# Optimization experiments

Hardware: AMD Instinct MI355X
Metric: run time of the kernel (lower is better)

## Reference

```python
import jax, jax.numpy as jnp
import numpy as np

EPS = 1e-5  # torch BatchNorm default

def _conv(x, w, pad):
    return jax.lax.conv_general_dilated(x, w, window_strides=(1, 1), padding=pad,
                                        dimension_numbers=('NCHW', 'OIHW', 'NCHW'))

def _bn(x, g, b, m, v):
    # eval-mode BatchNorm2d over channel axis 1 of NCHW
    scale = g / jnp.sqrt(v + EPS)
    return x * scale[None, :, None, None] + (b - m * scale)[None, :, None, None]

def _bn1d(x, g, b, m, v):
    scale = g / jnp.sqrt(v + EPS)
    return x * scale[None, :] + (b - m * scale)[None, :]

def _prelu(x, a):
    # torch PReLU with num_parameters=1 (scalar slope, init 0.25)
    return jnp.where(x >= 0, x, a * x)

def setup_inputs():
    key = jax.random.key(0)
    ks = jax.random.split(key, 10)
    B, H, W = 256, 600, 19
    C1, C2 = 40, 40
    x = jax.random.normal(ks[0], (B, H, W), jnp.float32)
    w1 = jax.random.normal(ks[1], (C1, 1, 29, 1), jnp.float32) * 0.1
    w2 = jax.random.normal(ks[2], (C2, C1, 1, 19), jnp.float32) * 0.1
    fc1_w = jax.random.uniform(ks[3], (80, 1560), jnp.float32, -0.005, 0.005)
    fc2_w = jax.random.uniform(ks[4], (2, 80), jnp.float32, -0.005, 0.005)
    def bn_params(k, n):
        k1, k2 = jax.random.split(k)
        return (jnp.ones((n,), jnp.float32), jnp.zeros((n,), jnp.float32),
                jax.random.normal(k1, (n,), jnp.float32) * 0.1,
                jax.random.uniform(k2, (n,), jnp.float32, 0.5, 1.5))
    bn1_g, bn1_b, bn1_m, bn1_v = bn_params(ks[5], C1)
    bn2_g, bn2_b, bn2_m, bn2_v = bn_params(ks[6], C2)
    bn3_g, bn3_b, bn3_m, bn3_v = bn_params(ks[7], 80)
    a1 = jnp.full((1,), 0.25, jnp.float32)
    a2 = jnp.full((1,), 0.25, jnp.float32)
    a3 = jnp.full((1,), 0.25, jnp.float32)
    return dict(x=x, w1=w1, bn1_g=bn1_g, bn1_b=bn1_b, bn1_m=bn1_m, bn1_v=bn1_v, a1=a1,
                w2=w2, bn2_g=bn2_g, bn2_b=bn2_b, bn2_m=bn2_m, bn2_v=bn2_v, a2=a2,
                fc1_w=fc1_w, bn3_g=bn3_g, bn3_b=bn3_b, bn3_m=bn3_m, bn3_v=bn3_v, a3=a3,
                fc2_w=fc2_w)

def reference(x, w1, bn1_g, bn1_b, bn1_m, bn1_v, a1,
              w2, bn2_g, bn2_b, bn2_m, bn2_v, a2,
              fc1_w, bn3_g, bn3_b, bn3_m, bn3_v, a3, fc2_w):
    h = x[:, None, :, :]                                  # [B,1,600,19]
    # conv1: inputs NOT binarized, weights sign-binarized
    h = _conv(h, jnp.sign(w1), [(14, 14), (0, 0)])         # [B,40,600,19]
    h = _prelu(_bn(h, bn1_g, bn1_b, bn1_m, bn1_v), a1)
    # conv2: inputs and weights binarized
    h = _conv(jnp.sign(h), jnp.sign(w2), [(0, 0), (0, 0)])  # [B,40,600,1]
    h = _prelu(_bn(h, bn2_g, bn2_b, bn2_m, bn2_v), a2)
    # AvgPool2d kernel (30,1) stride (15,1)
    h = jax.lax.reduce_window(h, 0.0, jax.lax.add, (1, 1, 30, 1), (1, 1, 15, 1), 'VALID') / 30.0  # [B,40,39,1]
    h = h.reshape(h.shape[0], -1)                          # [B,1560]
    # fc1: binarized input/weight; BatchNorm1d; PReLU; dropout is identity in eval
    h = jnp.sign(h) @ jnp.sign(fc1_w).T                    # [B,80]
    h = _prelu(_bn1d(h, bn3_g, bn3_b, bn3_m, bn3_v), a3)
    out = jnp.sign(h) @ jnp.sign(fc2_w).T                  # [B,2]
    return out
```

## Files before the change

### kernel.cpp

```cpp
#include <hip/hip_runtime.h>
#include <stdint.h>

#define B_ 256
#define H_ 600
#define W_ 19
#define C1_ 40
#define C2_ 40
#define KH_ 29
#define PAD_ 14
#define NW_ 760
#define NWORDS_ 12
#define NJ_ 39
#define FIN_ 1560
#define FOUT_ 80
#define FCW_ 25
#define XST2 329
#define HS_ 300

__device__ __forceinline__ float fsgn(float x){ return (x > 0.f) ? 1.f : ((x < 0.f) ? -1.f : 0.f); }
__device__ __forceinline__ int8_t isgn(float x){ return (int8_t)((x > 0.f) - (x < 0.f)); }

__global__ void k0_setup(const float* __restrict__ w1, const float* __restrict__ w2,
                         const float* __restrict__ fc1w, const float* __restrict__ fc2w,
                         const float* __restrict__ g1, const float* __restrict__ b1,
                         const float* __restrict__ m1, const float* __restrict__ v1,
                         const float* __restrict__ g2, const float* __restrict__ b2,
                         const float* __restrict__ m2, const float* __restrict__ v2,
                         const float* __restrict__ g3, const float* __restrict__ b3,
                         const float* __restrict__ m3, const float* __restrict__ v3,
                         float* __restrict__ w1s, uint64_t* __restrict__ w2m,
                         uint64_t* __restrict__ fc1p, int8_t* __restrict__ fc2s,
                         float* __restrict__ bnp)
{
  int tid = blockIdx.x * blockDim.x + threadIdx.x;
  int np  = gridDim.x * blockDim.x;
  int lane = threadIdx.x & 63;
  int gw   = tid >> 6;
  int nw   = np >> 6;

  for (int i = tid; i < C1_*KH_; i += np) w1s[i] = fsgn(w1[i]);

  for (int v = gw; v < C2_*NWORDS_; v += nw){
    int c2 = v / NWORDS_, wd = v % NWORDS_;
    int idx = wd*64 + lane;
    float val = 0.f;
    if (idx < NW_){
      int c1 = idx % 40, w = idx / 40;
      val = w2[c2*NW_ + c1*W_ + w];
    }
    unsigned long long m = __ballot(val > 0.f);
    if (lane == 0) w2m[c2*NWORDS_ + wd] = m;
  }
  for (int v = gw; v < FOUT_*2*FCW_; v += nw){
    int o = v / (2*FCW_), r = v % (2*FCW_);
    int neg = r / FCW_, wd = r % FCW_;
    int e = wd*64 + lane;
    float val = (e < FIN_) ? fc1w[o*FIN_ + e] : 0.f;
    unsigned long long m = __ballot(neg ? (val < 0.f) : (val > 0.f));
    if (lane == 0) fc1p[o*(2*FCW_) + r] = m;
  }
  for (int i = tid; i < 2*FOUT_; i += np) fc2s[i] = isgn(fc2w[i]);
  for (int i = tid; i < C1_; i += np){
    float s = __fdiv_rn(g1[i], __fsqrt_rn(__fadd_rn(v1[i], 1e-5f)));
    bnp[i] = s; bnp[40+i] = __fsub_rn(b1[i], __fmul_rn(m1[i], s));
  }
  for (int i = tid; i < C2_; i += np){
    float s = __fdiv_rn(g2[i], __fsqrt_rn(__fadd_rn(v2[i], 1e-5f)));
    bnp[80+i] = s; bnp[120+i] = __fsub_rn(b2[i], __fmul_rn(m2[i], s));
  }
  for (int i = tid; i < FOUT_; i += np){
    float s = __fdiv_rn(g3[i], __fsqrt_rn(__fadd_rn(v3[i], 1e-5f)));
    bnp[160+i] = s; bnp[240+i] = __fsub_rn(b3[i], __fmul_rn(m3[i], s));
  }
}

template<int T>
__device__ __forceinline__ float acc29(float (&xw)[29], float (&wt)[29]){
  float a = 0.f;
  #pragma unroll
  for (int k = 0; k < 29; ++k)
    a = __builtin_fmaf(wt[k], xw[(T + k) % 29], a);
  return a;
}

template<int T>
__device__ __forceinline__ void step1(float (&xw)[29], float (&wt)[29],
                                      const float* xck, ulonglong2* ob,
                                      float scale, float bias, int lane){
  xw[(T + 28) % 29] = xck[T + 28];
  float acc = acc29<T>(xw, wt);
  float z = __fadd_rn(__fmul_rn(acc, scale), bias);
  unsigned long long pp = __ballot(z > 0.f);
  unsigned long long nn = __ballot(z < 0.f);
  if (lane == 0){ ulonglong2 v; v.x = pp; v.y = pp | nn; ob[T] = v; }
}

#define S1(t) step1<t>(xw, wt, xck, ob, scale, bias, lane);

__global__ __launch_bounds__(768, 6) void k1_conv1(const float* __restrict__ x,
                                                   const float* __restrict__ w1s,
                                                   const float* __restrict__ bnp,
                                                   uint64_t* __restrict__ s1bits)
{
  __shared__ float xs[W_ * XST2];
  int b = blockIdx.x, t = blockIdx.y;
  int h0 = HS_ * t;
  const float* xb = x + (size_t)b * H_ * W_;
  for (int i = threadIdx.x; i < (HS_ + 28) * W_; i += 768){
    int r = i / W_, w = i % W_;
    int gh = h0 - PAD_ + r;
    xs[w*XST2 + r] = (gh >= 0 && gh < H_) ? xb[gh*W_ + w] : 0.f;
  }
  __syncthreads();

  int tid  = threadIdx.x;
  int lane = tid & 63, wave = tid >> 6;
  bool valid = (tid < NW_);
  int c1 = tid % 40;
  int w  = valid ? (tid / 40) : 18;

  float wt[KH_];
  #pragma unroll
  for (int k = 0; k < KH_; ++k) wt[k] = w1s[c1*KH_ + k];
  float scale = bnp[c1], bias = bnp[40 + c1];
  if (!valid){ scale = __builtin_nanf(""); bias = scale; }
  const float* xcol = &xs[w * XST2];

  float xw[29];
  #pragma unroll
  for (int s = 0; s < 28; ++s) xw[s] = xcol[s];

  ulonglong2* obase = (ulonglong2*)s1bits + ((size_t)(b*12 + wave) * H_ + h0);

  #pragma unroll 1
  for (int c = 0; c < 10; ++c){
    const float* xck = xcol + 29*c;
    ulonglong2* ob = obase + 29*c;
    S1(0)  S1(1)  S1(2)  S1(3)  S1(4)  S1(5)  S1(6)  S1(7)  S1(8)  S1(9)
    S1(10) S1(11) S1(12) S1(13) S1(14) S1(15) S1(16) S1(17) S1(18) S1(19)
    S1(20) S1(21) S1(22) S1(23) S1(24) S1(25) S1(26) S1(27) S1(28)
  }
  {
    const float* xck = xcol + 290;
    ulonglong2* ob = obase + 290;
    S1(0) S1(1) S1(2) S1(3) S1(4) S1(5) S1(6) S1(7) S1(8) S1(9)
  }
}

__global__ __launch_bounds__(640) void k2_conv2pool(const uint64_t* __restrict__ s1bits,
                                                    const uint64_t* __restrict__ w2m_g,
                                                    const float* __restrict__ bnp,
                                                    const float* __restrict__ a2p,
                                                    int8_t* __restrict__ sp)
{
  __shared__ float z[C2_][640];
  int b = blockIdx.x;
  int tid = threadIdx.x;
  int rowc = (tid < H_) ? tid : (H_ - 1);

  uint64_t Pv[NWORDS_], Mv[NWORDS_];
  const ulonglong2* sb = (const ulonglong2*)s1bits + (size_t)b * NWORDS_ * H_;
  #pragma unroll
  for (int wd = 0; wd < NWORDS_; ++wd){
    ulonglong2 pm = sb[(size_t)wd * H_ + rowc];
    Pv[wd] = pm.x; Mv[wd] = pm.y;
  }
  int nzv = 0;
  #pragma unroll
  for (int wd = 0; wd < NWORDS_; ++wd) nzv += __popcll(Mv[wd]);

  float alpha = a2p[0];
  #pragma unroll 2
  for (int c2 = 0; c2 < C2_; ++c2){
    int dsum = 0;
    #pragma unroll
    for (int wd = 0; wd < NWORDS_; ++wd)
      dsum += __popcll(Mv[wd] & (Pv[wd] ^ w2m_g[c2*NWORDS_ + wd]));
    int y = nzv - 2*dsum;
    float u = __fadd_rn(__fmul_rn((float)y, bnp[c2]), bnp[40 + c2]);
    z[c2][tid] = (u >= 0.f) ? u : __fmul_rn(alpha, u);
  }
  __syncthreads();

  for (int o = tid; o < C2_*NJ_; o += 640){
    int c2 = o / NJ_, j = o % NJ_;
    float s = 0.f;
    int base = 15*j;
    #pragma unroll
    for (int r = 0; r < 30; ++r) s = __fadd_rn(s, z[c2][base + r]);
    sp[(size_t)b*FIN_ + o] = (int8_t)((s > 0.f) - (s < 0.f));
  }
}

__global__ __launch_bounds__(128) void k3_fc(const int8_t* __restrict__ sp,
                                             const uint64_t* __restrict__ fc1p,
                                             const int8_t* __restrict__ fc2s,
                                             const float* __restrict__ bnp,
                                             const float* __restrict__ a3p,
                                             float* __restrict__ out)
{
  __shared__ uint64_t spP[FCW_], spN[FCW_];
  __shared__ int z3[FOUT_];
  int b = blockIdx.x;
  int lane = threadIdx.x & 63, wave = threadIdx.x >> 6;
  const int8_t* spb = sp + (size_t)b * FIN_;
  for (int wd = wave; wd < FCW_; wd += 2){
    int e = wd*64 + lane;
    int v = (e < FIN_) ? (int)spb[e] : 0;
    unsigned long long p = __ballot(v > 0);
    unsigned long long n = __ballot(v < 0);
    if (lane == 0){ spP[wd] = p; spN[wd] = n; }
  }
  __syncthreads();
  float alpha = a3p[0];
  if (threadIdx.x < FOUT_){
    int o = threadIdx.x;
    const uint64_t* wp = fc1p + o * (2*FCW_);
    int acc = 0;
    #pragma unroll
    for (int wd = 0; wd < FCW_; ++wd){
      uint64_t P = spP[wd], N = spN[wd];
      uint64_t WP = wp[wd], WN = wp[FCW_ + wd];
      acc += __popcll(P & WP) + __popcll(N & WN) - __popcll(P & WN) - __popcll(N & WP);
    }
    float u = __fadd_rn(__fmul_rn((float)acc, bnp[o]), bnp[80 + o]);
    float z = (u >= 0.f) ? u : __fmul_rn(alpha, u);
    z3[o] = (z > 0.f) - (z < 0.f);
  }
  __syncthreads();
  if (threadIdx.x < 2){
    int k = threadIdx.x;
    int acc = 0;
    for (int o = 0; o < FOUT_; ++o) acc += z3[o] * (int)fc2s[k * FOUT_ + o];
    out[b*2 + k] = (float)acc;
  }
}

extern "C" void kernel_launch(void* const* d_in, const int* in_sizes, int n_in,
                              void* d_out, int out_size, void* d_ws, size_t ws_size,
                              hipStream_t stream)
{
  const float* x    = (const float*)d_in[0];
  const float* w1   = (const float*)d_in[1];
  const float* g1   = (const float*)d_in[2];
  const float* b1   = (const float*)d_in[3];
  const float* m1   = (const float*)d_in[4];
  const float* v1   = (const float*)d_in[5];
  const float* a1   = (const float*)d_in[6];   (void)a1;
  const float* w2   = (const float*)d_in[7];
  const float* g2   = (const float*)d_in[8];
  const float* b2   = (const float*)d_in[9];
  const float* m2   = (const float*)d_in[10];
  const float* v2   = (const float*)d_in[11];
  const float* a2   = (const float*)d_in[12];
  const float* fc1w = (const float*)d_in[13];
  const float* g3   = (const float*)d_in[14];
  const float* b3   = (const float*)d_in[15];
  const float* m3   = (const float*)d_in[16];
  const float* v3   = (const float*)d_in[17];
  const float* a3   = (const float*)d_in[18];
  const float* fc2w = (const float*)d_in[19];

  char* ws = (char*)d_ws;
  uint64_t* s1bits = (uint64_t*)(ws);
  uint64_t* w2m    = (uint64_t*)(ws + 29491200);
  float*    w1s    = (float*)   (ws + 29495040);
  float*    bnp    = (float*)   (ws + 29499680);
  int8_t*   sp     = (int8_t*)  (ws + 29500960);
  uint64_t* fc1p   = (uint64_t*)(ws + 29900320);
  int8_t*   fc2s   = (int8_t*)  (ws + 29932320);

  k0_setup<<<dim3(128), dim3(256), 0, stream>>>(w1, w2, fc1w, fc2w,
                                                g1, b1, m1, v1,
                                                g2, b2, m2, v2,
                                                g3, b3, m3, v3,
                                                w1s, w2m, fc1p, fc2s, bnp);
  k1_conv1<<<dim3(B_, 2), dim3(768), 0, stream>>>(x, w1s, bnp, s1bits);
  k2_conv2pool<<<dim3(B_), dim3(640), 0, stream>>>(s1bits, w2m, bnp + 80, a2, sp);
  k3_fc<<<dim3(B_), dim3(128), 0, stream>>>(sp, fc1p, fc2s, bnp + 160, a3, (float*)d_out);
}
```

Baseline: 219.9 us.

## Fuse conv2/pool with FC layers and retile conv1 into smaller blocks

The conv2+pool kernel and the FC kernel are merged into one, so pooled signs are packed into bitmasks via ballot in shared memory and the int8 intermediate round-trip plus a launch are removed. Conv1 is retiled from 768-thread blocks over 300-row halves into 256-thread blocks over 150-row quarters across three wave groups. This gives more, smaller blocks for occupancy at the cost of more halo reloads. Opaque asm barriers are added on loads to stop the compiler rematerialising or reordering shared and weight loads.

```diff
diff --git a/kernel.cpp b/kernel.cpp
--- a/kernel.cpp
+++ b/kernel.cpp
@@ -14,8 +14,8 @@
 #define FIN_ 1560
 #define FOUT_ 80
 #define FCW_ 25
-#define XST2 329
-#define HS_ 300
+#define HS1 150
+#define XSTL 179
 
 __device__ __forceinline__ float fsgn(float x){ return (x > 0.f) ? 1.f : ((x < 0.f) ? -1.f : 0.f); }
 __device__ __forceinline__ int8_t isgn(float x){ return (int8_t)((x > 0.f) - (x < 0.f)); }
@@ -74,6 +74,8 @@
   }
 }
 
+__device__ __forceinline__ float opaque(float v){ asm volatile("" : "+v"(v)); return v; }
+
 template<int T>
 __device__ __forceinline__ float acc29(float (&xw)[29], float (&wt)[29]){
   float a = 0.f;
@@ -87,7 +89,7 @@
 __device__ __forceinline__ void step1(float (&xw)[29], float (&wt)[29],
                                       const float* xck, ulonglong2* ob,
                                       float scale, float bias, int lane){
-  xw[(T + 28) % 29] = xck[T + 28];
+  xw[(T + 28) % 29] = opaque(xck[T + 28]);
   float acc = acc29<T>(xw, wt);
   float z = __fadd_rn(__fmul_rn(acc, scale), bias);
   unsigned long long pp = __ballot(z > 0.f);
@@ -97,43 +99,44 @@
 
 #define S1(t) step1<t>(xw, wt, xck, ob, scale, bias, lane);
 
-__global__ __launch_bounds__(768, 6) void k1_conv1(const float* __restrict__ x,
+__global__ __launch_bounds__(256, 6) void k1_conv1(const float* __restrict__ x,
                                                    const float* __restrict__ w1s,
                                                    const float* __restrict__ bnp,
                                                    uint64_t* __restrict__ s1bits)
 {
-  __shared__ float xs[W_ * XST2];
-  int b = blockIdx.x, t = blockIdx.y;
-  int h0 = HS_ * t;
+  __shared__ float xs[W_ * XSTL];
+  int b = blockIdx.x, ht = blockIdx.y, g = blockIdx.z;
+  int h0 = HS1 * ht;
   const float* xb = x + (size_t)b * H_ * W_;
-  for (int i = threadIdx.x; i < (HS_ + 28) * W_; i += 768){
+  for (int i = threadIdx.x; i < (HS1 + 28) * W_; i += 256){
     int r = i / W_, w = i % W_;
     int gh = h0 - PAD_ + r;
-    xs[w*XST2 + r] = (gh >= 0 && gh < H_) ? xb[gh*W_ + w] : 0.f;
-  }
-  __syncthreads();
-
-  int tid  = threadIdx.x;
-  int lane = tid & 63, wave = tid >> 6;
-  bool valid = (tid < NW_);
-  int c1 = tid % 40;
-  int w  = valid ? (tid / 40) : 18;
+    xs[w*XSTL + r] = (gh >= 0 && gh < H_) ? xb[gh*W_ + w] : 0.f;
+  }
+  __syncthreads();
+
+  int lane = threadIdx.x & 63, wave = threadIdx.x >> 6;
+  int wd   = g*4 + wave;
+  int idx  = wd*64 + lane;
+  bool valid = (idx < NW_);
+  int c1 = idx % 40;
+  int w  = valid ? (idx / 40) : 18;
 
   float wt[KH_];
   #pragma unroll
-  for (int k = 0; k < KH_; ++k) wt[k] = w1s[c1*KH_ + k];
+  for (int k = 0; k < KH_; ++k) wt[k] = opaque(w1s[c1*KH_ + k]);
   float scale = bnp[c1], bias = bnp[40 + c1];
   if (!valid){ scale = __builtin_nanf(""); bias = scale; }
-  const float* xcol = &xs[w * XST2];
+  const float* xcol = &xs[w * XSTL];
 
   float xw[29];
   #pragma unroll
-  for (int s = 0; s < 28; ++s) xw[s] = xcol[s];
-
-  ulonglong2* obase = (ulonglong2*)s1bits + ((size_t)(b*12 + wave) * H_ + h0);
+  for (int s = 0; s < 28; ++s) xw[s] = opaque(xcol[s]);
+
+  ulonglong2* obase = (ulonglong2*)s1bits + ((size_t)(b*12 + wd) * H_ + h0);
 
   #pragma unroll 1
-  for (int c = 0; c < 10; ++c){
+  for (int c = 0; c < 5; ++c){
     const float* xck = xcol + 29*c;
     ulonglong2* ob = obase + 29*c;
     S1(0)  S1(1)  S1(2)  S1(3)  S1(4)  S1(5)  S1(6)  S1(7)  S1(8)  S1(9)
@@ -141,21 +144,27 @@
     S1(20) S1(21) S1(22) S1(23) S1(24) S1(25) S1(26) S1(27) S1(28)
   }
   {
-    const float* xck = xcol + 290;
-    ulonglong2* ob = obase + 290;
-    S1(0) S1(1) S1(2) S1(3) S1(4) S1(5) S1(6) S1(7) S1(8) S1(9)
-  }
-}
-
-__global__ __launch_bounds__(640) void k2_conv2pool(const uint64_t* __restrict__ s1bits,
-                                                    const uint64_t* __restrict__ w2m_g,
-                                                    const float* __restrict__ bnp,
-                                                    const float* __restrict__ a2p,
-                                                    int8_t* __restrict__ sp)
+    const float* xck = xcol + 145;
+    ulonglong2* ob = obase + 145;
+    S1(0) S1(1) S1(2) S1(3) S1(4)
+  }
+}
+
+__global__ __launch_bounds__(640) void k2_fused(const uint64_t* __restrict__ s1bits,
+                                                const uint64_t* __restrict__ w2m_g,
+                                                const uint64_t* __restrict__ fc1p,
+                                                const int8_t* __restrict__ fc2s,
+                                                const float* __restrict__ bnp,
+                                                const float* __restrict__ a2p,
+                                                const float* __restrict__ a3p,
+                                                float* __restrict__ out)
 {
   __shared__ float z[C2_][640];
+  __shared__ uint64_t spP[FCW_], spN[FCW_];
+  __shared__ int z3[FOUT_];
   int b = blockIdx.x;
   int tid = threadIdx.x;
+  int lane = tid & 63;
   int rowc = (tid < H_) ? tid : (H_ - 1);
 
   uint64_t Pv[NWORDS_], Mv[NWORDS_];
@@ -169,7 +178,7 @@
   #pragma unroll
   for (int wd = 0; wd < NWORDS_; ++wd) nzv += __popcll(Mv[wd]);
 
-  float alpha = a2p[0];
+  float alpha2 = a2p[0];
   #pragma unroll 2
   for (int c2 = 0; c2 < C2_; ++c2){
     int dsum = 0;
@@ -177,44 +186,30 @@
     for (int wd = 0; wd < NWORDS_; ++wd)
       dsum += __popcll(Mv[wd] & (Pv[wd] ^ w2m_g[c2*NWORDS_ + wd]));
     int y = nzv - 2*dsum;
-    float u = __fadd_rn(__fmul_rn((float)y, bnp[c2]), bnp[40 + c2]);
-    z[c2][tid] = (u >= 0.f) ? u : __fmul_rn(alpha, u);
-  }
-  __syncthreads();
-
-  for (int o = tid; o < C2_*NJ_; o += 640){
-    int c2 = o / NJ_, j = o % NJ_;
+    float u = __fadd_rn(__fmul_rn((float)y, bnp[80 + c2]), bnp[120 + c2]);
+    z[c2][tid] = (u >= 0.f) ? u : __fmul_rn(alpha2, u);
+  }
+  __syncthreads();
+
+  #pragma unroll 1
+  for (int ch = 0; ch < 3; ++ch){
+    int o = ch*640 + tid;
+    bool act = (o < FIN_);
+    int c2 = act ? (o / NJ_) : 0, j = act ? (o % NJ_) : 0;
+    int base = 15*j;
     float s = 0.f;
-    int base = 15*j;
     #pragma unroll
     for (int r = 0; r < 30; ++r) s = __fadd_rn(s, z[c2][base + r]);
-    sp[(size_t)b*FIN_ + o] = (int8_t)((s > 0.f) - (s < 0.f));
-  }
-}
-
-__global__ __launch_bounds__(128) void k3_fc(const int8_t* __restrict__ sp,
-                                             const uint64_t* __restrict__ fc1p,
-                                             const int8_t* __restrict__ fc2s,
-                                             const float* __restrict__ bnp,
-                                             const float* __restrict__ a3p,
-                                             float* __restrict__ out)
-{
-  __shared__ uint64_t spP[FCW_], spN[FCW_];
-  __shared__ int z3[FOUT_];
-  int b = blockIdx.x;
-  int lane = threadIdx.x & 63, wave = threadIdx.x >> 6;
-  const int8_t* spb = sp + (size_t)b * FIN_;
-  for (int wd = wave; wd < FCW_; wd += 2){
-    int e = wd*64 + lane;
-    int v = (e < FIN_) ? (int)spb[e] : 0;
-    unsigned long long p = __ballot(v > 0);
-    unsigned long long n = __ballot(v < 0);
-    if (lane == 0){ spP[wd] = p; spN[wd] = n; }
-  }
-  __syncthreads();
-  float alpha = a3p[0];
-  if (threadIdx.x < FOUT_){
-    int o = threadIdx.x;
+    unsigned long long pp = __ballot(act && (s > 0.f));
+    unsigned long long nn = __ballot(act && (s < 0.f));
+    int word = ch*10 + (tid >> 6);
+    if (lane == 0 && word < FCW_){ spP[word] = pp; spN[word] = nn; }
+  }
+  __syncthreads();
+
+  float alpha3 = a3p[0];
+  if (tid < FOUT_){
+    int o = tid;
     const uint64_t* wp = fc1p + o * (2*FCW_);
     int acc = 0;
     #pragma unroll
@@ -223,16 +218,15 @@
       uint64_t WP = wp[wd], WN = wp[FCW_ + wd];
       acc += __popcll(P & WP) + __popcll(N & WN) - __popcll(P & WN) - __popcll(N & WP);
     }
-    float u = __fadd_rn(__fmul_rn((float)acc, bnp[o]), bnp[80 + o]);
-    float z = (u >= 0.f) ? u : __fmul_rn(alpha, u);
-    z3[o] = (z > 0.f) - (z < 0.f);
-  }
-  __syncthreads();
-  if (threadIdx.x < 2){
-    int k = threadIdx.x;
+    float u = __fadd_rn(__fmul_rn((float)acc, bnp[160 + o]), bnp[240 + o]);
+    float zz = (u >= 0.f) ? u : __fmul_rn(alpha3, u);
+    z3[o] = (zz > 0.f) - (zz < 0.f);
+  }
+  __syncthreads();
+  if (tid < 2){
     int acc = 0;
-    for (int o = 0; o < FOUT_; ++o) acc += z3[o] * (int)fc2s[k * FOUT_ + o];
-    out[b*2 + k] = (float)acc;
+    for (int o = 0; o < FOUT_; ++o) acc += z3[o] * (int)fc2s[tid * FOUT_ + o];
+    out[b*2 + tid] = (float)acc;
   }
 }
 
@@ -266,16 +260,15 @@
   uint64_t* w2m    = (uint64_t*)(ws + 29491200);
   float*    w1s    = (float*)   (ws + 29495040);
   float*    bnp    = (float*)   (ws + 29499680);
-  int8_t*   sp     = (int8_t*)  (ws + 29500960);
-  uint64_t* fc1p   = (uint64_t*)(ws + 29900320);
-  int8_t*   fc2s   = (int8_t*)  (ws + 29932320);
+  uint64_t* fc1p   = (uint64_t*)(ws + 29500960);
+  int8_t*   fc2s   = (int8_t*)  (ws + 29532960);
 
   k0_setup<<<dim3(128), dim3(256), 0, stream>>>(w1, w2, fc1w, fc2w,
                                                 g1, b1, m1, v1,
                                                 g2, b2, m2, v2,
                                                 g3, b3, m3, v3,
                                                 w1s, w2m, fc1p, fc2s, bnp);
-  k1_conv1<<<dim3(B_, 2), dim3(768), 0, stream>>>(x, w1s, bnp, s1bits);
-  k2_conv2pool<<<dim3(B_), dim3(640), 0, stream>>>(s1bits, w2m, bnp + 80, a2, sp);
-  k3_fc<<<dim3(B_), dim3(128), 0, stream>>>(sp, fc1p, fc2s, bnp + 160, a3, (float*)d_out);
-}
+  k1_conv1<<<dim3(B_, 4, 3), dim3(256), 0, stream>>>(x, w1s, bnp, s1bits);
+  k2_fused<<<dim3(B_), dim3(640), 0, stream>>>(s1bits, w2m, fc1p, fc2s, bnp,
+                                               a2, a3, (float*)d_out);
+}
```

Measured after the change: 220.9 us. About the same (+0.4%).
